# Optimization experiments

Measured on AMD Instinct MI355X. Metric: run time of the kernel, lower is better.

## Reference

```python
import jax, jax.numpy as jnp
import numpy as np

H = 12  # num_heads


def rotate_half(x):
    x1, x2 = jnp.split(x, 2, axis=-1)
    return jnp.concatenate([-x2, x1], axis=-1)


def setup_inputs() -> dict:
    key = jax.random.key(0)
    ks = jax.random.split(key, 8)
    B, N, C = 4, 2048, 768
    num_special = 5
    Ns = N - num_special
    D = C // H
    x = jax.random.normal(ks[0], (B, N, C), dtype=jnp.float32)
    rope_cos = jax.random.uniform(ks[1], (Ns, D), dtype=jnp.float32)
    rope_sin = jax.random.uniform(ks[2], (Ns, D), dtype=jnp.float32)
    W_qkv = jax.random.normal(ks[3], (C, 3 * C), dtype=jnp.float32) * (C ** -0.5)
    b_qkv = jax.random.normal(ks[4], (3 * C,), dtype=jnp.float32) * 0.02
    W_proj = jax.random.normal(ks[5], (C, C), dtype=jnp.float32) * (C ** -0.5)
    b_proj = jax.random.normal(ks[6], (C,), dtype=jnp.float32) * 0.02
    return {"x": x, "rope_cos": rope_cos, "rope_sin": rope_sin,
            "W_qkv": W_qkv, "b_qkv": b_qkv, "W_proj": W_proj, "b_proj": b_proj,
            "num_special": num_special}


def reference(x, rope_cos, rope_sin, W_qkv, b_qkv, W_proj, b_proj, num_special):
    B, N, C = x.shape
    D = C // H
    scale = D ** -0.5
    qkv = (x @ W_qkv + b_qkv).reshape(B, N, 3, H, D)
    qkv = jnp.transpose(qkv, (2, 0, 3, 1, 4))  # [3, B, H, N, D]
    q, k, v = qkv[0], qkv[1], qkv[2]
    # partial RoPE: special tokens untouched, spatial tokens rotated
    q_spec, q_spat = q[:, :, :num_special], q[:, :, num_special:]
    k_spec, k_spat = k[:, :, :num_special], k[:, :, num_special:]
    q_spat = q_spat * rope_cos + rotate_half(q_spat) * rope_sin
    k_spat = k_spat * rope_cos + rotate_half(k_spat) * rope_sin
    q = jnp.concatenate([q_spec, q_spat], axis=2)
    k = jnp.concatenate([k_spec, k_spat], axis=2)
    attn = jnp.einsum('bhqd,bhkd->bhqk', q, k) * scale  # [B,H,N,N]
    attn = jax.nn.softmax(attn, axis=-1)
    out = jnp.einsum('bhqk,bhkd->bhqd', attn, v)  # [B,H,N,D]
    out = jnp.transpose(out, (0, 2, 1, 3)).reshape(B, N, C)
    return out @ W_proj + b_proj
```

## Files before the change

kernel.cpp:

```cpp
#include <hip/hip_runtime.h>
#include <stdint.h>

typedef unsigned short u16;
typedef __bf16 bf16x8 __attribute__((ext_vector_type(8)));
typedef __bf16 bf16x2 __attribute__((ext_vector_type(2)));
typedef short s16x4 __attribute__((ext_vector_type(4)));
typedef float f32x4 __attribute__((ext_vector_type(4)));

typedef __attribute__((address_space(1))) void gvoid_t;
typedef __attribute__((address_space(3))) void lvoid_t;

struct alignas(16) U128 { uint32_t x, y, z, w; };
struct alignas(16) F128 { float x, y, z, w; };
struct alignas(8)  U64v { uint32_t x, y; };

__device__ __forceinline__ void gld16(const u16* g, u16* lds) {
  __builtin_amdgcn_global_load_lds((gvoid_t*)const_cast<u16*>(g),
                                   (lvoid_t*)lds, 16, 0, 0);
}

__device__ __forceinline__ u16 f2bf(float f) {
  uint32_t u = __builtin_bit_cast(uint32_t, f);
  u += 0x7FFFu + ((u >> 16) & 1u);
  return (u16)(u >> 16);
}
__device__ __forceinline__ float bf2f(u16 h) {
  return __builtin_bit_cast(float, (uint32_t)h << 16);
}
__device__ __forceinline__ bf16x8 ldfrag(const u16* p) {
  U128 u = *reinterpret_cast<const U128*>(p);
  return __builtin_bit_cast(bf16x8, u);
}
__device__ __forceinline__ uint32_t pkbf(float a, float b) {
  bf16x2 v;
  v[0] = (__bf16)a;
  v[1] = (__bf16)b;
  return __builtin_bit_cast(uint32_t, v);
}

__device__ __forceinline__ float EXP2(float x) { return __builtin_amdgcn_exp2f(x); }

__global__ void cvt_f32_bf16(const float* __restrict__ in, u16* __restrict__ out) {
  int i = (blockIdx.x * 256 + threadIdx.x) * 4;
  F128 v = *reinterpret_cast<const F128*>(in + i);
  U64v o;
  o.x = (uint32_t)f2bf(v.x) | ((uint32_t)f2bf(v.y) << 16);
  o.y = (uint32_t)f2bf(v.z) | ((uint32_t)f2bf(v.w) << 16);
  *reinterpret_cast<U64v*>(out + i) = o;
}

__global__ void transpose_cvt(const float* __restrict__ W, u16* __restrict__ Wt,
                              int K, int N) {
  __shared__ float T[32][33];
  const int n0 = blockIdx.x * 32, k0 = blockIdx.y * 32;
  const int tid = threadIdx.x;
#pragma unroll
  for (int i = 0; i < 4; ++i) {
    int e = i * 256 + tid, r = e >> 5, c = e & 31;
    T[r][c] = W[(size_t)(k0 + r) * N + n0 + c];
  }
  __syncthreads();
#pragma unroll
  for (int i = 0; i < 4; ++i) {
    int e = i * 256 + tid, r = e >> 5, c = e & 31;
    Wt[(size_t)(n0 + r) * K + k0 + c] = f2bf(T[c][r]);
  }
}


#define GEMM3_BODY(A_, Bt_, K_)                                                        \
  extern __shared__ u16 smem[];                                                        \
  u16* Asm = smem;                               \
  u16* Bsm = smem + 3 * 8192;                   \
  const int tid = threadIdx.x;                                                         \
  const int wave = tid >> 6, lane = tid & 63;                                          \
  const int quad = lane >> 4, l16 = lane & 15;                                         \
  const int wm = wave >> 2, wn = wave & 3;                                             \
  const int m0 = blockIdx.y * 128, n0 = blockIdx.x * 256;                              \
  const int lrow = lane >> 3;                                                          \
  const int csrc = (lane & 7) ^ lrow;                   \
  const int ar0 = wave * 16;                \
  const int br0 = wave * 32;                \
  const u16* Ag = (A_) + (size_t)(m0 + ar0 + lrow) * (K_) + csrc * 8;                  \
  const u16* Bg = (Bt_) + (size_t)(n0 + br0 + lrow) * (K_) + csrc * 8;                 \
  f32x4 acc[4][4];                                                                     \
  _Pragma("unroll")                                                                    \
  for (int i = 0; i < 4; ++i)                                                          \
    _Pragma("unroll")                                                                  \
    for (int j = 0; j < 4; ++j) acc[i][j] = (f32x4){0.f, 0.f, 0.f, 0.f};               \
  STG3(0, 0);                                                                          \
  STG3(1, 1);                                                                          \
  const int arow = wm * 64 + l16;                                                      \
  const int brow = wn * 64 + l16;                                                      \
  const int swz = l16 & 7;                                                             \
  for (int kt = 0; kt < 12; ++kt) {                                                    \
    if (kt < 11) asm volatile("s_waitcnt vmcnt(6)" ::: "memory");                      \
    else         asm volatile("s_waitcnt vmcnt(0)" ::: "memory");                      \
    __builtin_amdgcn_s_barrier();                                                      \
    __builtin_amdgcn_sched_barrier(0);                                                 \
    if (kt + 2 < 12) STG3(kt + 2, (kt + 2) % 3);                                       \
    const u16* Ab = Asm + (kt % 3) * 8192;                                             \
    const u16* Bb = Bsm + (kt % 3) * 16384;                                            \
    _Pragma("unroll")                                                                  \
    for (int kk = 0; kk < 2; ++kk) {                                                   \
      bf16x8 af[4], bfr[4];                                                            \
      _Pragma("unroll")                                                                \
      for (int rb = 0; rb < 4; ++rb)                                                   \
        af[rb] = ldfrag(Ab + (arow + rb * 16) * 64 + ((((kk << 2) | quad) ^ swz) << 3)); \
      _Pragma("unroll")                                                                \
      for (int cb = 0; cb < 4; ++cb)                                                   \
        bfr[cb] = ldfrag(Bb + (brow + cb * 16) * 64 + ((((kk << 2) | quad) ^ swz) << 3)); \
      __builtin_amdgcn_s_setprio(1);                                                   \
      _Pragma("unroll")                                                                \
      for (int rb = 0; rb < 4; ++rb)                                                   \
        _Pragma("unroll")                                                              \
        for (int cb = 0; cb < 4; ++cb)                                                 \
          acc[rb][cb] = __builtin_amdgcn_mfma_f32_16x16x32_bf16(af[rb], bfr[cb], acc[rb][cb], 0, 0, 0); \
      __builtin_amdgcn_s_setprio(0);                                                   \
    }                                                                                  \
  }

#define STG3(kt_, s_) do {                                                             \
    const u16* As_ = Ag + (kt_) * 64;                                                  \
    const u16* Bs_ = Bg + (kt_) * 64;                                                  \
    u16* Ad = Asm + (s_) * 8192 + ar0 * 64;                                            \
    u16* Bd = Bsm + (s_) * 16384 + br0 * 64;                                           \
    gld16(As_, Ad);                gld16(As_ + 8 * KDIM, Ad + 512);                    \
    gld16(Bs_, Bd);                gld16(Bs_ + 8 * KDIM, Bd + 512);                    \
    gld16(Bs_ + 16 * KDIM, Bd + 1024); gld16(Bs_ + 24 * KDIM, Bd + 1536);              \
  } while (0)

__global__ __launch_bounds__(512, 2)
void gemm_bt(const u16* __restrict__ A, const u16* __restrict__ Bt,
             const float* __restrict__ bias, float* __restrict__ C,
             int M, int N, int Karg) {
  const int KDIM = 768;
  (void)M; (void)Karg;
  GEMM3_BODY(A, Bt, KDIM)
#pragma unroll
  for (int cb = 0; cb < 4; ++cb) {
    int col = n0 + wn * 64 + cb * 16 + l16;
    float bv = bias[col];
#pragma unroll
    for (int rb = 0; rb < 4; ++rb) {
#pragma unroll
      for (int r = 0; r < 4; ++r) {
        int row = m0 + wm * 64 + rb * 16 + quad * 4 + r;
        C[(size_t)row * N + col] = acc[rb][cb][r] + bv;
      }
    }
  }
}

__global__ __launch_bounds__(512, 2)
void gemm_qkv_rope(const u16* __restrict__ A, const u16* __restrict__ Bt,
                   const float* __restrict__ bias,
                   const float* __restrict__ cosT, const float* __restrict__ sinT,
                   const int* __restrict__ nsp,
                   u16* __restrict__ Qo, u16* __restrict__ Ko, u16* __restrict__ Vto) {
  const int KDIM = 768;
  GEMM3_BODY(A, Bt, KDIM)
  const int sec = blockIdx.x / 3;
  const int gcol0 = n0 + wn * 64;
  const int hh = (gcol0 >> 6) % 12;
  const int bb = m0 >> 11;
  const int nbase = m0 & 2047;
  const int bh = bb * 12 + hh;
  const int num_special = nsp[0];
  const float QS = 0.125f * 1.4426950408889634f;

  if (sec < 2) {
    u16* outp = sec ? Ko : Qo;
    const float qs = sec ? 1.0f : QS;
#pragma unroll
    for (int cbp = 0; cbp < 2; ++cbp) {
      const int d1 = cbp * 16 + l16;
      const int d2 = d1 + 32;
      const float bv1 = bias[gcol0 + d1];
      const float bv2 = bias[gcol0 + d2];
#pragma unroll
      for (int rb = 0; rb < 4; ++rb) {
#pragma unroll
        for (int r = 0; r < 4; ++r) {
          const int n = nbase + wm * 64 + rb * 16 + quad * 4 + r;
          float v1 = acc[rb][cbp][r] + bv1;
          float v2 = acc[rb][cbp + 2][r] + bv2;
          float o1, o2;
          if (n < num_special) {
            o1 = v1; o2 = v2;
          } else {
            int ns = n - num_special;
            float c1 = cosT[ns * 64 + d1], s1 = sinT[ns * 64 + d1];
            float c2 = cosT[ns * 64 + d2], s2 = sinT[ns * 64 + d2];
            o1 = v1 * c1 - v2 * s1;
            o2 = v2 * c2 + v1 * s2;
          }
          size_t ob = ((size_t)bh * 2048 + n) * 64;
          outp[ob + d1] = f2bf(o1 * qs);
          outp[ob + d2] = f2bf(o2 * qs);
        }
      }
    }
  } else {
#pragma unroll
    for (int cb = 0; cb < 4; ++cb) {
      const int d = cb * 16 + l16;
      const float bv = bias[gcol0 + d];
#pragma unroll
      for (int rb = 0; rb < 4; ++rb) {
        const int nr = nbase + wm * 64 + rb * 16 + quad * 4;
        U64v o;
        o.x = (uint32_t)f2bf(acc[rb][cb][0] + bv) |
              ((uint32_t)f2bf(acc[rb][cb][1] + bv) << 16);
        o.y = (uint32_t)f2bf(acc[rb][cb][2] + bv) |
              ((uint32_t)f2bf(acc[rb][cb][3] + bv) << 16);
        *(U64v*)&Vto[((size_t)bh * 64 + d) * 2048 + nr] = o;
      }
    }
  }
}

__global__ __launch_bounds__(256, 3)
void attn(const u16* __restrict__ Q, const u16* __restrict__ Kg,
          const u16* __restrict__ Vt, u16* __restrict__ Out) {
  __shared__ u16 smem[2 * 8192];
  __shared__ float invS[64];
  const int tid = threadIdx.x;
  const int wave = tid >> 6, lane = tid & 63;
  const int quad = lane >> 4, l16 = lane & 15;
  const int idx = blockIdx.x;
  const int bh = idx % 48, qt = idx / 48;
  const int b = bh / 12, h = bh % 12;
  const u16* Qb = Q + (size_t)bh * 2048 * 64;
  const u16* Kb = Kg + (size_t)bh * 2048 * 64;
  const u16* Vb = Vt + (size_t)bh * 64 * 2048;
  const int wkey0 = wave * 16;

  const int lrow = lane >> 3;
  const int lch  = (lane & 7) ^ (lrow & 7);
  const int r0a = wave * 8;
  const int r0b = 32 + wave * 8;
  const int ksrc_a = (r0a + lrow) * 64 + lch * 8;
  const int ksrc_b = (r0b + lrow) * 64 + lch * 8;
  const size_t vsrc_a = (size_t)(r0a + lrow) * 2048 + lch * 8;
  const size_t vsrc_b = (size_t)(r0b + lrow) * 2048 + lch * 8;

  const int krd = (wkey0 + l16) * 64 + ((quad ^ (l16 & 7)) << 3);
  int vrd[4];
#pragma unroll
  for (int db = 0; db < 4; ++db)
    vrd[db] = (db * 16 + l16) * 64 +
              ((((wave << 1) | (quad >> 1)) ^ (l16 & 7)) << 3) + (quad & 1) * 4;

#define STAGE_A(kt_, s_)                                                      \
  do {                                                                        \
    u16* Kd = smem + (s_) * 8192;                                             \
    u16* Vd = Kd + 4096;                                                      \
    const u16* Ksrc = Kb + (size_t)(kt_) * 4096;                              \
    const u16* Vsrc = Vb + (kt_) * 64;                                        \
    gld16(Ksrc + ksrc_a, Kd + r0a * 64);                                      \
    gld16(Ksrc + ksrc_b, Kd + r0b * 64);                                      \
    gld16(Vsrc + vsrc_a, Vd + r0a * 64);                                      \
    gld16(Vsrc + vsrc_b, Vd + r0b * 64);                                      \
  } while (0)

  bf16x8 qf[4][2];
#pragma unroll
  for (int m = 0; m < 4; ++m) {
    const u16* qp = Qb + (size_t)(qt * 64 + m * 16 + l16) * 64 + quad * 8;
    qf[m][0] = ldfrag(qp);
    qf[m][1] = ldfrag(qp + 32);
  }

  f32x4 oacc[4][4];
#pragma unroll
  for (int m = 0; m < 4; ++m)
#pragma unroll
    for (int db = 0; db < 4; ++db) oacc[m][db] = (f32x4){0.f, 0.f, 0.f, 0.f};
  float psum[4] = {0.f, 0.f, 0.f, 0.f};

  STAGE_A(0, 0);
  STAGE_A(1, 1);
  __syncthreads();

  s16x4 pf[4];
  U64v  vfc[4];
  {
    const u16* Ksh = smem;
    const u16* Vsh = smem + 4096;
    bf16x8 ka0 = ldfrag(Ksh + krd);
    bf16x8 ka1 = ldfrag(Ksh + (krd ^ 32));
#pragma unroll
    for (int db = 0; db < 4; ++db) vfc[db] = *(const U64v*)(Vsh + vrd[db]);
#pragma unroll
    for (int m = 0; m < 4; ++m) {
      f32x4 st = (f32x4){0.f, 0.f, 0.f, 0.f};
      st = __builtin_amdgcn_mfma_f32_16x16x32_bf16(ka0, qf[m][0], st, 0, 0, 0);
      st = __builtin_amdgcn_mfma_f32_16x16x32_bf16(ka1, qf[m][1], st, 0, 0, 0);
      float p0 = EXP2(st[0]), p1 = EXP2(st[1]), p2 = EXP2(st[2]), p3 = EXP2(st[3]);
      psum[m] += (p0 + p1) + (p2 + p3);
      U64v pd; pd.x = pkbf(p0, p1); pd.y = pkbf(p2, p3);
      pf[m] = __builtin_bit_cast(s16x4, pd);
    }
  }
  __syncthreads();

  for (int kt = 0; kt < 31; ++kt) {
    const int cur = kt & 1, nxt = cur ^ 1;
    const u16* Kshn = smem + nxt * 8192;
    const u16* Vshn = Kshn + 4096;
    bf16x8 kn0 = ldfrag(Kshn + krd);
    bf16x8 kn1 = ldfrag(Kshn + (krd ^ 32));
    U64v vfn[4];
#pragma unroll
    for (int db = 0; db < 4; ++db) vfn[db] = *(const U64v*)(Vshn + vrd[db]);

    if (kt < 30) STAGE_A(kt + 2, cur);

    s16x4 pfn[4];
#pragma unroll
    for (int m = 0; m < 4; ++m) {
      f32x4 st = (f32x4){0.f, 0.f, 0.f, 0.f};
      st = __builtin_amdgcn_mfma_f32_16x16x32_bf16(kn0, qf[m][0], st, 0, 0, 0);
      st = __builtin_amdgcn_mfma_f32_16x16x32_bf16(kn1, qf[m][1], st, 0, 0, 0);
#pragma unroll
      for (int db = 0; db < 4; ++db)
        oacc[m][db] = __builtin_amdgcn_mfma_f32_16x16x16bf16_1k(pf[m], __builtin_bit_cast(s16x4, vfc[db]), oacc[m][db], 0, 0, 0);
      float p0 = EXP2(st[0]), p1 = EXP2(st[1]), p2 = EXP2(st[2]), p3 = EXP2(st[3]);
      psum[m] += (p0 + p1) + (p2 + p3);
      U64v pd; pd.x = pkbf(p0, p1); pd.y = pkbf(p2, p3);
      pfn[m] = __builtin_bit_cast(s16x4, pd);
    }
    __syncthreads();
#pragma unroll
    for (int m = 0; m < 4; ++m) pf[m] = pfn[m];
#pragma unroll
    for (int db = 0; db < 4; ++db) vfc[db] = vfn[db];
  }

#pragma unroll
  for (int m = 0; m < 4; ++m)
#pragma unroll
    for (int db = 0; db < 4; ++db)
      oacc[m][db] = __builtin_amdgcn_mfma_f32_16x16x16bf16_1k(pf[m], __builtin_bit_cast(s16x4, vfc[db]), oacc[m][db], 0, 0, 0);
#undef STAGE_A

#pragma unroll
  for (int m = 0; m < 4; ++m) {
    psum[m] += __shfl_xor(psum[m], 16, 64);
    psum[m] += __shfl_xor(psum[m], 32, 64);
  }
  __syncthreads();
  float* LS = (float*)smem;
  if (quad == 0) {
#pragma unroll
    for (int m = 0; m < 4; ++m) LS[wave * 64 + m * 16 + l16] = psum[m];
  }
  __syncthreads();
  if (tid < 64) {
    float tot = LS[tid] + LS[64 + tid] + LS[128 + tid] + LS[192 + tid];
    invS[tid] = 1.0f / tot;
  }

  float* OR = (float*)smem;
  const int q = tid >> 2;
  const int d0 = (tid & 3) * 4;
  const size_t obase = ((size_t)(b * 2048 + qt * 64 + q)) * 768 + h * 64 + d0;
#pragma unroll
  for (int db = 0; db < 4; ++db) {
    __syncthreads();
#pragma unroll
    for (int m = 0; m < 4; ++m)
#pragma unroll
      for (int r = 0; r < 4; ++r)
        OR[(wave * 64 + m * 16 + quad * 4 + r) * 18 + l16] = oacc[m][db][r];
    __syncthreads();
    float s0 = 0.f, s1 = 0.f, s2 = 0.f, s3 = 0.f;
#pragma unroll
    for (int w = 0; w < 4; ++w) {
      const float* p = &OR[(w * 64 + q) * 18 + d0];
      s0 += p[0]; s1 += p[1]; s2 += p[2]; s3 += p[3];
    }
    float iv = invS[q];
    U64v o;
    o.x = (uint32_t)f2bf(s0 * iv) | ((uint32_t)f2bf(s1 * iv) << 16);
    o.y = (uint32_t)f2bf(s2 * iv) | ((uint32_t)f2bf(s3 * iv) << 16);
    *(U64v*)&Out[obase + db * 16] = o;
  }
}

extern "C" void kernel_launch(void* const* d_in, const int* in_sizes, int n_in,
                              void* d_out, int out_size, void* d_ws, size_t ws_size,
                              hipStream_t stream) {
  (void)in_sizes; (void)n_in; (void)out_size; (void)ws_size;
  const float* x        = (const float*)d_in[0];
  const float* rope_cos = (const float*)d_in[1];
  const float* rope_sin = (const float*)d_in[2];
  const float* W_qkv    = (const float*)d_in[3];
  const float* b_qkv    = (const float*)d_in[4];
  const float* W_proj   = (const float*)d_in[5];
  const float* b_proj   = (const float*)d_in[6];
  const int*   nsp      = (const int*)d_in[7];
  float* out = (float*)d_out;

  char* ws = (char*)d_ws;
  u16* Xb   = (u16*)(ws);
  u16* Wqkt = (u16*)(ws + 12582912);
  u16* Wpt  = (u16*)(ws + 16121856);
  u16* Qb   = (u16*)(ws + 55050240);
  u16* Kb   = (u16*)(ws + 67633152);
  u16* Vtb  = (u16*)(ws + 80216064);
  u16* att  = (u16*)(ws + 92798976);

  static bool attr_done = false;
  if (!attr_done) {
    hipFuncSetAttribute(reinterpret_cast<const void*>(gemm_qkv_rope),
                        hipFuncAttributeMaxDynamicSharedMemorySize, 147456);
    hipFuncSetAttribute(reinterpret_cast<const void*>(gemm_bt),
                        hipFuncAttributeMaxDynamicSharedMemorySize, 147456);
    attr_done = true;
  }

  cvt_f32_bf16<<<6144, 256, 0, stream>>>(x, Xb);
  transpose_cvt<<<dim3(72, 24), 256, 0, stream>>>(W_qkv, Wqkt, 768, 2304);
  transpose_cvt<<<dim3(24, 24), 256, 0, stream>>>(W_proj, Wpt, 768, 768);
  gemm_qkv_rope<<<dim3(9, 64), 512, 147456, stream>>>(Xb, Wqkt, b_qkv, rope_cos, rope_sin,
                                                      nsp, Qb, Kb, Vtb);
  attn<<<1536, 256, 0, stream>>>(Qb, Kb, Vtb, att);
  gemm_bt<<<dim3(3, 64), 512, 147456, stream>>>(att, Wpt, b_proj, out, 8192, 768, 768);
}
```

Baseline: 261.6 us.

## Retile GEMMs to 128x128 blocks with 256 threads, swizzled block order, split attention launch

```diff
diff --git a/kernel.cpp b/kernel.cpp
--- a/kernel.cpp
+++ b/kernel.cpp
@@ -68,100 +68,104 @@
 }
 
 
-#define GEMM3_BODY(A_, Bt_, K_)                                                        \
-  extern __shared__ u16 smem[];                                                        \
-  u16* Asm = smem;                               \
-  u16* Bsm = smem + 3 * 8192;                   \
-  const int tid = threadIdx.x;                                                         \
-  const int wave = tid >> 6, lane = tid & 63;                                          \
-  const int quad = lane >> 4, l16 = lane & 15;                                         \
-  const int wm = wave >> 2, wn = wave & 3;                                             \
-  const int m0 = blockIdx.y * 128, n0 = blockIdx.x * 256;                              \
-  const int lrow = lane >> 3;                                                          \
-  const int csrc = (lane & 7) ^ lrow;                   \
-  const int ar0 = wave * 16;                \
-  const int br0 = wave * 32;                \
-  const u16* Ag = (A_) + (size_t)(m0 + ar0 + lrow) * (K_) + csrc * 8;                  \
-  const u16* Bg = (Bt_) + (size_t)(n0 + br0 + lrow) * (K_) + csrc * 8;                 \
-  f32x4 acc[4][4];                                                                     \
-  _Pragma("unroll")                                                                    \
-  for (int i = 0; i < 4; ++i)                                                          \
-    _Pragma("unroll")                                                                  \
-    for (int j = 0; j < 4; ++j) acc[i][j] = (f32x4){0.f, 0.f, 0.f, 0.f};               \
-  STG3(0, 0);                                                                          \
-  STG3(1, 1);                                                                          \
-  const int arow = wm * 64 + l16;                                                      \
-  const int brow = wn * 64 + l16;                                                      \
-  const int swz = l16 & 7;                                                             \
-  for (int kt = 0; kt < 12; ++kt) {                                                    \
-    if (kt < 11) asm volatile("s_waitcnt vmcnt(6)" ::: "memory");                      \
-    else         asm volatile("s_waitcnt vmcnt(0)" ::: "memory");                      \
-    __builtin_amdgcn_s_barrier();                                                      \
-    __builtin_amdgcn_sched_barrier(0);                                                 \
-    if (kt + 2 < 12) STG3(kt + 2, (kt + 2) % 3);                                       \
-    const u16* Ab = Asm + (kt % 3) * 8192;                                             \
-    const u16* Bb = Bsm + (kt % 3) * 16384;                                            \
-    _Pragma("unroll")                                                                  \
-    for (int kk = 0; kk < 2; ++kk) {                                                   \
-      bf16x8 af[4], bfr[4];                                                            \
-      _Pragma("unroll")                                                                \
-      for (int rb = 0; rb < 4; ++rb)                                                   \
-        af[rb] = ldfrag(Ab + (arow + rb * 16) * 64 + ((((kk << 2) | quad) ^ swz) << 3)); \
-      _Pragma("unroll")                                                                \
-      for (int cb = 0; cb < 4; ++cb)                                                   \
-        bfr[cb] = ldfrag(Bb + (brow + cb * 16) * 64 + ((((kk << 2) | quad) ^ swz) << 3)); \
-      __builtin_amdgcn_s_setprio(1);                                                   \
-      _Pragma("unroll")                                                                \
-      for (int rb = 0; rb < 4; ++rb)                                                   \
-        _Pragma("unroll")                                                              \
-        for (int cb = 0; cb < 4; ++cb)                                                 \
-          acc[rb][cb] = __builtin_amdgcn_mfma_f32_16x16x32_bf16(af[rb], bfr[cb], acc[rb][cb], 0, 0, 0); \
-      __builtin_amdgcn_s_setprio(0);                                                   \
-    }                                                                                  \
-  }
-
-#define STG3(kt_, s_) do {                                                             \
-    const u16* As_ = Ag + (kt_) * 64;                                                  \
-    const u16* Bs_ = Bg + (kt_) * 64;                                                  \
-    u16* Ad = Asm + (s_) * 8192 + ar0 * 64;                                            \
-    u16* Bd = Bsm + (s_) * 16384 + br0 * 64;                                           \
-    gld16(As_, Ad);                gld16(As_ + 8 * KDIM, Ad + 512);                    \
-    gld16(Bs_, Bd);                gld16(Bs_ + 8 * KDIM, Bd + 512);                    \
-    gld16(Bs_ + 16 * KDIM, Bd + 1024); gld16(Bs_ + 24 * KDIM, Bd + 1536);              \
+#define GEMM_PIPE(A_, Bt_, KD_, NKT_)                                                \
+  const int tid = threadIdx.x;                                                       \
+  const int wave = tid >> 6, lane = tid & 63;                                        \
+  const int quad = lane >> 4, l16 = lane & 15;                                       \
+  const int m0 = by * 128, n0 = bx * 128;                                            \
+  const int wr = (wave & 1) * 64, wc = (wave >> 1) * 64;                             \
+  f32x4 acc[4][4];                                                                   \
+  _Pragma("unroll")                                                                  \
+  for (int i = 0; i < 4; ++i)                                                        \
+    _Pragma("unroll")                                                                \
+    for (int j = 0; j < 4; ++j) acc[i][j] = (f32x4){0.f, 0.f, 0.f, 0.f};             \
+  const int c0 = wave * 128 + lane;                                                  \
+  const int row0 = c0 >> 2, kq0 = c0 & 3;                                            \
+  const int c1 = c0 + 64;                                                            \
+  const int row1 = c1 >> 2, kq1 = c1 & 3;                                            \
+  const u16* Ag0 = (A_) + (size_t)(m0 + row0) * (KD_) + kq0 * 8;                     \
+  const u16* Ag1 = (A_) + (size_t)(m0 + row1) * (KD_) + kq1 * 8;                     \
+  const u16* Bg0 = (Bt_) + (size_t)(n0 + row0) * (KD_) + kq0 * 8;                    \
+  const u16* Bg1 = (Bt_) + (size_t)(n0 + row1) * (KD_) + kq1 * 8;                    \
+  STG(0, 0);                                                                         \
+  STG(1, 1);                                                                         \
+  for (int t = 0; t < (NKT_); ++t) {                                                 \
+    __builtin_amdgcn_sched_barrier(0);                                               \
+    if (t < (NKT_) - 1) asm volatile("s_waitcnt vmcnt(4)" ::: "memory");             \
+    else                asm volatile("s_waitcnt vmcnt(0)" ::: "memory");             \
+    __builtin_amdgcn_sched_barrier(0);                                               \
+    __builtin_amdgcn_s_barrier();                                                    \
+    __builtin_amdgcn_sched_barrier(0);                                               \
+    if (t + 2 < (NKT_)) STG(t + 2, (t + 2) % 3);                                     \
+    const u16* Ab = Asl + (t % 3) * 4096;                                            \
+    const u16* Bb = Bsl + (t % 3) * 4096;                                            \
+    bf16x8 af[4], bfr[4];                                                            \
+    _Pragma("unroll")                                                                \
+    for (int rb = 0; rb < 4; ++rb)                                                   \
+      af[rb] = ldfrag(&Ab[(wr + rb * 16 + l16) * 32 + quad * 8]);                    \
+    _Pragma("unroll")                                                                \
+    for (int cb = 0; cb < 4; ++cb)                                                   \
+      bfr[cb] = ldfrag(&Bb[(wc + cb * 16 + l16) * 32 + quad * 8]);                   \
+    __builtin_amdgcn_s_setprio(1);                                                   \
+    _Pragma("unroll")                                                                \
+    for (int rb = 0; rb < 4; ++rb)                                                   \
+      _Pragma("unroll")                                                              \
+      for (int cb = 0; cb < 4; ++cb)                                                 \
+        acc[rb][cb] = __builtin_amdgcn_mfma_f32_16x16x32_bf16(                       \
+            af[rb], bfr[cb], acc[rb][cb], 0, 0, 0);                                  \
+    __builtin_amdgcn_s_setprio(0);                                                   \
+  }
+
+#define STG(t_, s_)                                                                  \
+  do {                                                                               \
+    const int k0_ = (t_) * 32;                                                       \
+    gld16(Ag0 + k0_, &Asl[(s_) * 4096 + wave * 1024]);                               \
+    gld16(Bg0 + k0_, &Bsl[(s_) * 4096 + wave * 1024]);                               \
+    gld16(Ag1 + k0_, &Asl[(s_) * 4096 + wave * 1024 + 512]);                         \
+    gld16(Bg1 + k0_, &Bsl[(s_) * 4096 + wave * 1024 + 512]);                         \
   } while (0)
 
-__global__ __launch_bounds__(512, 2)
+__global__ __launch_bounds__(256, 3)
 void gemm_bt(const u16* __restrict__ A, const u16* __restrict__ Bt,
              const float* __restrict__ bias, float* __restrict__ C,
              int M, int N, int Karg) {
-  const int KDIM = 768;
   (void)M; (void)Karg;
-  GEMM3_BODY(A, Bt, KDIM)
+  __shared__ u16 Asl[3 * 4096];
+  __shared__ u16 Bsl[3 * 4096];
+  const int orig = blockIdx.y * 6 + blockIdx.x;
+  const int swz = (orig % 8) * 48 + orig / 8;
+  const int bx = swz % 6, by = swz / 6;
+  GEMM_PIPE(A, Bt, 768, 24)
 #pragma unroll
   for (int cb = 0; cb < 4; ++cb) {
-    int col = n0 + wn * 64 + cb * 16 + l16;
+    int col = n0 + wc + cb * 16 + l16;
     float bv = bias[col];
 #pragma unroll
     for (int rb = 0; rb < 4; ++rb) {
 #pragma unroll
       for (int r = 0; r < 4; ++r) {
-        int row = m0 + wm * 64 + rb * 16 + quad * 4 + r;
+        int row = m0 + wr + rb * 16 + quad * 4 + r;
         C[(size_t)row * N + col] = acc[rb][cb][r] + bv;
       }
     }
   }
 }
 
-__global__ __launch_bounds__(512, 2)
+__global__ __launch_bounds__(256, 3)
 void gemm_qkv_rope(const u16* __restrict__ A, const u16* __restrict__ Bt,
                    const float* __restrict__ bias,
                    const float* __restrict__ cosT, const float* __restrict__ sinT,
                    const int* __restrict__ nsp,
                    u16* __restrict__ Qo, u16* __restrict__ Ko, u16* __restrict__ Vto) {
-  const int KDIM = 768;
-  GEMM3_BODY(A, Bt, KDIM)
-  const int sec = blockIdx.x / 3;
-  const int gcol0 = n0 + wn * 64;
+  __shared__ u16 Asl[3 * 4096];
+  __shared__ u16 Bsl[3 * 4096];
+  const int orig = blockIdx.y * 18 + blockIdx.x;
+  const int swz = (orig % 8) * 144 + orig / 8;
+  const int bx = swz % 18, by = swz / 18;
+  GEMM_PIPE(A, Bt, 768, 24)
+
+  const int sec = bx / 6;
+  const int gcol0 = n0 + wc;
   const int hh = (gcol0 >> 6) % 12;
   const int bb = m0 >> 11;
   const int nbase = m0 & 2047;
@@ -182,7 +186,7 @@
       for (int rb = 0; rb < 4; ++rb) {
 #pragma unroll
         for (int r = 0; r < 4; ++r) {
-          const int n = nbase + wm * 64 + rb * 16 + quad * 4 + r;
+          const int n = nbase + wr + rb * 16 + quad * 4 + r;
           float v1 = acc[rb][cbp][r] + bv1;
           float v2 = acc[rb][cbp + 2][r] + bv2;
           float o1, o2;
@@ -208,7 +212,7 @@
       const float bv = bias[gcol0 + d];
 #pragma unroll
       for (int rb = 0; rb < 4; ++rb) {
-        const int nr = nbase + wm * 64 + rb * 16 + quad * 4;
+        const int nr = nbase + wr + rb * 16 + quad * 4;
         U64v o;
         o.x = (uint32_t)f2bf(acc[rb][cb][0] + bv) |
               ((uint32_t)f2bf(acc[rb][cb][1] + bv) << 16);
@@ -222,14 +226,14 @@
 
 __global__ __launch_bounds__(256, 3)
 void attn(const u16* __restrict__ Q, const u16* __restrict__ Kg,
-          const u16* __restrict__ Vt, u16* __restrict__ Out) {
-  __shared__ u16 smem[2 * 8192];
+          const u16* __restrict__ Vt, u16* __restrict__ Out, int qt0) {
+  __shared__ u16 smem2[2 * 8192];
   __shared__ float invS[64];
   const int tid = threadIdx.x;
   const int wave = tid >> 6, lane = tid & 63;
   const int quad = lane >> 4, l16 = lane & 15;
   const int idx = blockIdx.x;
-  const int bh = idx % 48, qt = idx / 48;
+  const int bh = idx % 48, qt = idx / 48 + qt0;
   const int b = bh / 12, h = bh % 12;
   const u16* Qb = Q + (size_t)bh * 2048 * 64;
   const u16* Kb = Kg + (size_t)bh * 2048 * 64;
@@ -254,7 +258,7 @@
 
 #define STAGE_A(kt_, s_)                                                      \
   do {                                                                        \
-    u16* Kd = smem + (s_) * 8192;                                             \
+    u16* Kd = smem2 + (s_) * 8192;                                            \
     u16* Vd = Kd + 4096;                                                      \
     const u16* Ksrc = Kb + (size_t)(kt_) * 4096;                              \
     const u16* Vsrc = Vb + (kt_) * 64;                                        \
@@ -286,8 +290,8 @@
   s16x4 pf[4];
   U64v  vfc[4];
   {
-    const u16* Ksh = smem;
-    const u16* Vsh = smem + 4096;
+    const u16* Ksh = smem2;
+    const u16* Vsh = smem2 + 4096;
     bf16x8 ka0 = ldfrag(Ksh + krd);
     bf16x8 ka1 = ldfrag(Ksh + (krd ^ 32));
 #pragma unroll
@@ -307,7 +311,7 @@
 
   for (int kt = 0; kt < 31; ++kt) {
     const int cur = kt & 1, nxt = cur ^ 1;
-    const u16* Kshn = smem + nxt * 8192;
+    const u16* Kshn = smem2 + nxt * 8192;
     const u16* Vshn = Kshn + 4096;
     bf16x8 kn0 = ldfrag(Kshn + krd);
     bf16x8 kn1 = ldfrag(Kshn + (krd ^ 32));
@@ -351,7 +355,7 @@
     psum[m] += __shfl_xor(psum[m], 32, 64);
   }
   __syncthreads();
-  float* LS = (float*)smem;
+  float* LS = (float*)smem2;
   if (quad == 0) {
 #pragma unroll
     for (int m = 0; m < 4; ++m) LS[wave * 64 + m * 16 + l16] = psum[m];
@@ -362,7 +366,7 @@
     invS[tid] = 1.0f / tot;
   }
 
-  float* OR = (float*)smem;
+  float* OR = (float*)smem2;
   const int q = tid >> 2;
   const int d0 = (tid & 3) * 4;
   const size_t obase = ((size_t)(b * 2048 + qt * 64 + q)) * 768 + h * 64 + d0;
@@ -412,20 +416,12 @@
   u16* Vtb  = (u16*)(ws + 80216064);
   u16* att  = (u16*)(ws + 92798976);
 
-  static bool attr_done = false;
-  if (!attr_done) {
-    hipFuncSetAttribute(reinterpret_cast<const void*>(gemm_qkv_rope),
-                        hipFuncAttributeMaxDynamicSharedMemorySize, 147456);
-    hipFuncSetAttribute(reinterpret_cast<const void*>(gemm_bt),
-                        hipFuncAttributeMaxDynamicSharedMemorySize, 147456);
-    attr_done = true;
-  }
-
   cvt_f32_bf16<<<6144, 256, 0, stream>>>(x, Xb);
   transpose_cvt<<<dim3(72, 24), 256, 0, stream>>>(W_qkv, Wqkt, 768, 2304);
   transpose_cvt<<<dim3(24, 24), 256, 0, stream>>>(W_proj, Wpt, 768, 768);
-  gemm_qkv_rope<<<dim3(9, 64), 512, 147456, stream>>>(Xb, Wqkt, b_qkv, rope_cos, rope_sin,
-                                                      nsp, Qb, Kb, Vtb);
-  attn<<<1536, 256, 0, stream>>>(Qb, Kb, Vtb, att);
-  gemm_bt<<<dim3(3, 64), 512, 147456, stream>>>(att, Wpt, b_proj, out, 8192, 768, 768);
-}
+  gemm_qkv_rope<<<dim3(18, 64), 256, 0, stream>>>(Xb, Wqkt, b_qkv, rope_cos, rope_sin,
+                                                  nsp, Qb, Kb, Vtb);
+  attn<<<768, 256, 0, stream>>>(Qb, Kb, Vtb, att, 0);
+  attn<<<768, 256, 0, stream>>>(Qb, Kb, Vtb, att, 16);
+  gemm_bt<<<dim3(6, 64), 256, 0, stream>>>(att, Wpt, b_proj, out, 8192, 768, 768);
+}
```

Result: faster. 248.9 us (-4.9%).
